# Kernel tuning notes

Hardware: AMD Instinct MI355X
Metric: run time of the kernel (lower is better)

The kernel has to match this reference:

```python
import jax, jax.numpy as jnp
import numpy as np

N_HEADS = 16
ROPE_BASE = 10000.0

def rotate_half(x):
    x1, x2 = jnp.split(x, 2, axis=-1)
    return jnp.concatenate([-x2, x1], axis=-1)

def rope_cos_sin(seq_len, head_dim, dtype):
    inv_freq = 1.0 / (ROPE_BASE ** (jnp.arange(0, head_dim, 2, dtype=jnp.float32) / head_dim))
    t = jnp.arange(seq_len, dtype=jnp.float32)
    freqs = jnp.einsum('i,j->ij', t, inv_freq)           # [S, hd/2]
    emb = jnp.concatenate([freqs, freqs], axis=-1)        # [S, hd]
    return jnp.cos(emb).astype(dtype), jnp.sin(emb).astype(dtype)

def setup_inputs() -> dict:
    key = jax.random.key(0)
    ks = jax.random.split(key, 5)
    B, S, D = 2, 2048, 2048
    x = jax.random.normal(ks[0], (B, S, D), dtype=jnp.float32)
    Wq = jax.random.normal(ks[1], (D, D), dtype=jnp.float32) * (D ** -0.5)
    Wk = jax.random.normal(ks[2], (D, D), dtype=jnp.float32) * (D ** -0.5)
    Wv = jax.random.normal(ks[3], (D, D), dtype=jnp.float32) * (D ** -0.5)
    Wo = jax.random.normal(ks[4], (D, D), dtype=jnp.float32) * (D ** -0.5)
    return {'x': x, 'Wq': Wq, 'Wk': Wk, 'Wv': Wv, 'Wo': Wo}

def reference(x, Wq, Wk, Wv, Wo):
    B, S, D = x.shape
    H = N_HEADS
    hd = D // H
    scale = hd ** -0.5
    # projections (torch Linear: x @ W.T), split heads -> [B, H, S, hd]
    def proj(W):
        return (x @ W.T).reshape(B, S, H, hd).transpose(0, 2, 1, 3)
    q, k, v = proj(Wq), proj(Wk), proj(Wv)
    # RoPE
    cos, sin = rope_cos_sin(S, hd, x.dtype)               # [S, hd]
    cos = cos[None, None, :, :]
    sin = sin[None, None, :, :]
    q = q * cos + rotate_half(q) * sin
    k = k * cos + rotate_half(k) * sin
    # scores + causal mask + fp32 softmax
    scores = jnp.einsum('bhqd,bhkd->bhqk', q, k) * scale
    causal = jnp.triu(jnp.ones((S, S), dtype=bool), k=1)  # True above diag
    scores = jnp.where(causal[None, None, :, :], -jnp.inf, scores)
    attn = jax.nn.softmax(scores.astype(jnp.float32), axis=-1).astype(q.dtype)
    out = jnp.einsum('bhqk,bhkd->bhqd', attn, v)
    out = out.transpose(0, 2, 1, 3).reshape(B, S, D)
    return out @ Wo.T
```

## Files before the change

### kernel.cpp

```cpp
#include <hip/hip_runtime.h>
#include <hip/hip_bf16.h>
#include <math.h>

#define BB 2
#define SS 2048
#define DD 2048
#define HH 16
#define HD 128
#define MM (BB * SS)
#define SCALE 0.08838834764831845f

typedef __attribute__((ext_vector_type(8))) __bf16 bf16x8;
typedef __attribute__((ext_vector_type(4))) float f32x4;
typedef __attribute__((ext_vector_type(8))) unsigned short ushort8v;

__device__ __forceinline__ float bf2f(unsigned short u) {
    union { unsigned int u; float f; } x;
    x.u = ((unsigned int)u) << 16;
    return x.f;
}
__device__ __forceinline__ unsigned short f2bf(float f) {
    union { float f; unsigned int u; } x;
    x.f = f;
    unsigned int r = x.u + 0x7FFFu + ((x.u >> 16) & 1u);
    return (unsigned short)(r >> 16);
}

__global__ __launch_bounds__(256) void cast_f32_bf16(const float* __restrict__ src,
                                                     unsigned short* __restrict__ dst,
                                                     int n4) {
    int i = blockIdx.x * 256 + threadIdx.x;
    if (i >= n4) return;
    float4 v = ((const float4*)src)[i];
    ushort4 o;
    o.x = f2bf(v.x); o.y = f2bf(v.y); o.z = f2bf(v.z); o.w = f2bf(v.w);
    ((ushort4*)dst)[i] = o;
}

__global__ __launch_bounds__(64) void rope_table_kernel(float* __restrict__ cost,
                                                        float* __restrict__ sint) {
    int s = blockIdx.x;
    int i = threadIdx.x;
    float inv = powf(10000.0f, -((float)(2 * i) / 128.0f));
    float ang = (float)s * inv;
    cost[s * 64 + i] = cosf(ang);
    sint[s * 64 + i] = sinf(ang);
}

#define GEMM_BODY(A_, W_, m0_, n0_, K_, ACC_)                                      \
    for (int k0 = 0; k0 < (K_); k0 += 32) {                                        \
        __syncthreads();                                                           \
        _Pragma("unroll")                                                          \
        for (int i = 0; i < 2; ++i) {                                              \
            int c = 2 * w + i;                                                     \
            int row = c * 16 + (l >> 2);                                           \
            const unsigned short* ga = (A_) + (size_t)((m0_) + row) * (K_) + k0 + (l & 3) * 8; \
            __builtin_amdgcn_global_load_lds(                                      \
                (const __attribute__((address_space(1))) unsigned int*)ga,         \
                (__attribute__((address_space(3))) unsigned int*)(As + c * 512),   \
                16, 0, 0);                                                         \
            const unsigned short* gb = (W_) + (size_t)((n0_) + row) * (K_) + k0 + (l & 3) * 8; \
            __builtin_amdgcn_global_load_lds(                                      \
                (const __attribute__((address_space(1))) unsigned int*)gb,         \
                (__attribute__((address_space(3))) unsigned int*)(Bs + c * 512),   \
                16, 0, 0);                                                         \
        }                                                                          \
        __syncthreads();                                                           \
        bf16x8 af[4], bfr[4];                                                      \
        _Pragma("unroll")                                                          \
        for (int i = 0; i < 4; ++i) {                                              \
            af[i]  = *(const bf16x8*)&As[(wr + i * 16 + rlane) * 32 + g * 8];      \
            bfr[i] = *(const bf16x8*)&Bs[(wc + i * 16 + rlane) * 32 + g * 8];      \
        }                                                                          \
        _Pragma("unroll")                                                          \
        for (int i = 0; i < 4; ++i)                                                \
            _Pragma("unroll")                                                      \
            for (int j = 0; j < 4; ++j)                                            \
                ACC_[i][j] = __builtin_amdgcn_mfma_f32_16x16x32_bf16(af[i], bfr[j], ACC_[i][j], 0, 0, 0); \
    }

__global__ __launch_bounds__(256) void gemm_qkv(const unsigned short* __restrict__ A,
                                                const unsigned short* __restrict__ Wc,
                                                unsigned short* __restrict__ qkv) {
    __shared__ unsigned short As[128 * 32];
    __shared__ unsigned short Bs[128 * 32];
    int t = threadIdx.x, w = t >> 6, l = t & 63;
    int rlane = l & 15, g = l >> 4;
    int flat = (int)blockIdx.y * 48 + (int)blockIdx.x;
    int swz = (flat & 7) * 192 + (flat >> 3);
    int n0 = (swz % 48) * 128;
    int m0 = (swz / 48) * 128;
    int wr = (w >> 1) * 64, wc = (w & 1) * 64;
    f32x4 acc[4][4] = {};
    GEMM_BODY(A, Wc, m0, n0, 2048, acc)
    unsigned short* base = qkv + (size_t)(n0 >> 11) * ((size_t)MM * DD);
    int nc0 = n0 & 2047;
#pragma unroll
    for (int i = 0; i < 4; ++i)
#pragma unroll
        for (int r = 0; r < 4; ++r) {
            int row = m0 + wr + i * 16 + g * 4 + r;
#pragma unroll
            for (int j = 0; j < 4; ++j) {
                int col = nc0 + wc + j * 16 + rlane;
                base[(size_t)row * DD + col] = f2bf(acc[i][j][r]);
            }
        }
}

__global__ __launch_bounds__(256) void gemm_out(const unsigned short* __restrict__ A,
                                                const unsigned short* __restrict__ W,
                                                float* __restrict__ C) {
    __shared__ unsigned short As[128 * 32];
    __shared__ unsigned short Bs[128 * 32];
    int t = threadIdx.x, w = t >> 6, l = t & 63;
    int rlane = l & 15, g = l >> 4;
    int flat = (int)blockIdx.y * 16 + (int)blockIdx.x;
    int swz = (flat & 7) * 64 + (flat >> 3);
    int n0 = (swz % 16) * 128;
    int m0 = (swz / 16) * 128;
    int wr = (w >> 1) * 64, wc = (w & 1) * 64;
    f32x4 acc[4][4] = {};
    GEMM_BODY(A, W, m0, n0, 2048, acc)
#pragma unroll
    for (int i = 0; i < 4; ++i)
#pragma unroll
        for (int r = 0; r < 4; ++r) {
            int row = m0 + wr + i * 16 + g * 4 + r;
#pragma unroll
            for (int j = 0; j < 4; ++j) {
                int col = n0 + wc + j * 16 + rlane;
                C[(size_t)row * DD + col] = acc[i][j][r];
            }
        }
}

__global__ __launch_bounds__(256) void rope_apply_kernel(unsigned short* __restrict__ arr,
                                                         const float* __restrict__ cost,
                                                         const float* __restrict__ sint) {
    int idx = blockIdx.x * 256 + threadIdx.x;
    int i4 = (idx & 15) * 4;
    int h = (idx >> 4) & 15;
    int row = idx >> 8;
    int s = row & (SS - 1);
    float4 c  = *(const float4*)&cost[s * 64 + i4];
    float4 sn = *(const float4*)&sint[s * 64 + i4];
    size_t p0 = (size_t)row * DD + h * HD + i4;
    ushort4 lo = *(ushort4*)&arr[p0];
    ushort4 hi = *(ushort4*)&arr[p0 + 64];
    ushort4 olo, ohi;
    olo.x = f2bf(bf2f(lo.x) * c.x - bf2f(hi.x) * sn.x);
    olo.y = f2bf(bf2f(lo.y) * c.y - bf2f(hi.y) * sn.y);
    olo.z = f2bf(bf2f(lo.z) * c.z - bf2f(hi.z) * sn.z);
    olo.w = f2bf(bf2f(lo.w) * c.w - bf2f(hi.w) * sn.w);
    ohi.x = f2bf(bf2f(hi.x) * c.x + bf2f(lo.x) * sn.x);
    ohi.y = f2bf(bf2f(hi.y) * c.y + bf2f(lo.y) * sn.y);
    ohi.z = f2bf(bf2f(hi.z) * c.z + bf2f(lo.z) * sn.z);
    ohi.w = f2bf(bf2f(hi.w) * c.w + bf2f(lo.w) * sn.w);
    *(ushort4*)&arr[p0] = olo;
    *(ushort4*)&arr[p0 + 64] = ohi;
}

__global__ __launch_bounds__(256, 2) void mfma_attn(const unsigned short* __restrict__ qm,
                                                    const unsigned short* __restrict__ km,
                                                    const unsigned short* __restrict__ vm,
                                                    unsigned short* __restrict__ om) {
    __shared__ unsigned short Ks[2][64 * 128];
    __shared__ unsigned short Vt[2][128 * 64];
    __shared__ unsigned short Ps[4][16 * 40];

    int t = threadIdx.x;
    int w = t >> 6;
    int l = t & 63;
    int l15 = l & 15;
    int g = l >> 4;

    int pj = blockIdx.x;
    int h = blockIdx.y;
    int b = blockIdx.z;
    size_t bbase = (size_t)b * SS * DD + (size_t)h * HD;

    int vk0 = 2 * (t >> 3);
    int vd8 = t & 7;
    int cbase = (l15 >> 2) & 3;
    int gsw = (g ^ (l15 & 3)) * 8;

    auto stage_k = [&](int kt2, int buf) {
#pragma unroll
        for (int s = 0; s < 4; ++s) {
            int row = w * 16 + s * 4 + (l >> 4);
            int c = ((l >> 2) & 3) ^ s;
            int gg = (l & 3) ^ (l >> 4);
            const unsigned short* ga = km + bbase +
                (size_t)(kt2 * 64 + row) * DD + c * 32 + gg * 8;
            __builtin_amdgcn_global_load_lds(
                (const __attribute__((address_space(1))) unsigned int*)ga,
                (__attribute__((address_space(3))) unsigned int*)(&Ks[buf][(w * 16 + s * 4) * 128]),
                16, 0, 0);
        }
    };

    ushort8v va[2], vb[2];
    auto load_v = [&](int kt2) {
        const unsigned short* vsrc = vm + bbase + (size_t)(kt2 * 64 + vk0) * DD + vd8 * 8;
        va[0] = *(const ushort8v*)(vsrc);
        vb[0] = *(const ushort8v*)(vsrc + DD);
        va[1] = *(const ushort8v*)(vsrc + 64);
        vb[1] = *(const ushort8v*)(vsrc + DD + 64);
    };
    auto write_v = [&](int buf) {
#pragma unroll
        for (int i = 0; i < 2; ++i)
#pragma unroll
            for (int j = 0; j < 8; ++j) {
                int d = (vd8 + 8 * i) * 8 + j;
                int swz = (vk0 >> 3) ^ ((d >> 3) & 7);
                unsigned int pack = (unsigned int)va[i][j] | ((unsigned int)vb[i][j] << 16);
                *(unsigned int*)&Vt[buf][d * 64 + swz * 8 + (vk0 & 7)] = pack;
            }
    };

#pragma unroll 1
    for (int half = 0; half < 2; ++half) {
        int qt = half ? pj : (31 - pj);
        int q0 = qt * 64;

        bf16x8 qf[4];
        {
            int qrow = q0 + w * 16 + l15;
#pragma unroll
            for (int c = 0; c < 4; ++c)
                qf[c] = *(const bf16x8*)(qm + bbase + (size_t)qrow * DD + c * 32 + g * 8);
        }

        f32x4 acc_o[8] = {};
        float m_ = -INFINITY;
        float l_ = 0.0f;
        int nt = qt + 1;

        stage_k(0, 0);
        load_v(0);
        write_v(0);
        __syncthreads();

        for (int kt = 0; kt < nt; ++kt) {
            int cur = kt & 1;
            bool pref = (kt + 1 < nt);
            if (pref) {
                stage_k(kt + 1, cur ^ 1);
                load_v(kt + 1);
            }

            f32x4 s_[4] = {};
#pragma unroll
            for (int c = 0; c < 4; ++c) {
                int coff = ((c ^ cbase) * 32) + gsw;
#pragma unroll
                for (int kg = 0; kg < 4; ++kg) {
                    bf16x8 kf = *(const bf16x8*)&Ks[cur][(kg * 16 + l15) * 128 + coff];
                    s_[kg] = __builtin_amdgcn_mfma_f32_16x16x32_bf16(kf, qf[c], s_[kg], 0, 0, 0);
                }
            }

            float p[16];
            int qrel = w * 16 + l15;
            bool diag = (kt == qt);
#pragma unroll
            for (int kg = 0; kg < 4; ++kg)
#pragma unroll
                for (int r = 0; r < 4; ++r) {
                    float sv = s_[kg][r] * SCALE;
                    if (diag && (kg * 16 + g * 4 + r > qrel)) sv = -INFINITY;
                    p[kg * 4 + r] = sv;
                }
            float mt01 = fmaxf(fmaxf(p[0], p[1]), fmaxf(p[2], p[3]));
            float mt23 = fmaxf(fmaxf(p[4], p[5]), fmaxf(p[6], p[7]));
            float mt45 = fmaxf(fmaxf(p[8], p[9]), fmaxf(p[10], p[11]));
            float mt67 = fmaxf(fmaxf(p[12], p[13]), fmaxf(p[14], p[15]));
            float mt = fmaxf(fmaxf(mt01, mt23), fmaxf(mt45, mt67));
            mt = fmaxf(mt, __shfl_xor(mt, 16));
            mt = fmaxf(mt, __shfl_xor(mt, 32));
            if (!__all(mt - m_ <= 8.0f)) {
                float mnew = fmaxf(m_, mt);
                float alpha = __expf(m_ - mnew);
                float ar[4];
#pragma unroll
                for (int r = 0; r < 4; ++r) ar[r] = __shfl(alpha, 4 * g + r);
#pragma unroll
                for (int dg = 0; dg < 8; ++dg)
#pragma unroll
                    for (int r = 0; r < 4; ++r) acc_o[dg][r] *= ar[r];
                l_ *= alpha;
                m_ = mnew;
            }
            float ps = 0.0f;
#pragma unroll
            for (int n = 0; n < 16; ++n) {
                p[n] = __expf(p[n] - m_);
                ps += p[n];
            }
            ps += __shfl_xor(ps, 16);
            ps += __shfl_xor(ps, 32);
            l_ += ps;

#pragma unroll
            for (int ks = 0; ks < 2; ++ks) {
#pragma unroll
                for (int kh = 0; kh < 2; ++kh) {
                    int kg = 2 * ks + kh;
                    union { __bf16 hv[4]; uint2 u2; } pk;
#pragma unroll
                    for (int r = 0; r < 4; ++r) pk.hv[r] = (__bf16)p[kg * 4 + r];
                    *(uint2*)&Ps[w][l15 * 40 + kh * 16 + g * 4] = pk.u2;
                }
                bf16x8 pf = *(const bf16x8*)&Ps[w][l15 * 40 + g * 8];
#pragma unroll
                for (int dg = 0; dg < 8; ++dg) {
                    int d = dg * 16 + l15;
                    int swz = (ks * 4 + g) ^ ((d >> 3) & 7);
                    bf16x8 vf = *(const bf16x8*)&Vt[cur][d * 64 + swz * 8];
                    acc_o[dg] = __builtin_amdgcn_mfma_f32_16x16x32_bf16(pf, vf, acc_o[dg], 0, 0, 0);
                }
            }

            if (pref) write_v(cur ^ 1);
            __syncthreads();
        }

        float lr[4];
#pragma unroll
        for (int r = 0; r < 4; ++r) lr[r] = 1.0f / __shfl(l_, 4 * g + r);
#pragma unroll
        for (int dg = 0; dg < 8; ++dg)
#pragma unroll
            for (int r = 0; r < 4; ++r) {
                int qrow2 = q0 + w * 16 + g * 4 + r;
                om[bbase + (size_t)qrow2 * DD + dg * 16 + l15] =
                    f2bf(acc_o[dg][r] * lr[r]);
            }
    }
}

extern "C" void kernel_launch(void* const* d_in, const int* in_sizes, int n_in,
                              void* d_out, int out_size, void* d_ws, size_t ws_size,
                              hipStream_t stream) {
    const float* x  = (const float*)d_in[0];
    const float* Wq = (const float*)d_in[1];
    const float* Wk = (const float*)d_in[2];
    const float* Wv = (const float*)d_in[3];
    const float* Wo = (const float*)d_in[4];
    float* out = (float*)d_out;

    char* ws = (char*)d_ws;
    const size_t MD = (size_t)MM * DD;
    const size_t WN = (size_t)DD * DD;
    unsigned short* qb   = (unsigned short*)(ws);
    unsigned short* kb   = (unsigned short*)(ws + 2 * MD);
    unsigned short* vb   = (unsigned short*)(ws + 4 * MD);
    unsigned short* ctxb = (unsigned short*)(ws + 6 * MD);
    unsigned short* xb   = (unsigned short*)(ws + 8 * MD);
    unsigned short* wqb  = (unsigned short*)(ws + 10 * MD);
    unsigned short* wkb  = (unsigned short*)(ws + 10 * MD + 2 * WN);
    unsigned short* wvb  = (unsigned short*)(ws + 10 * MD + 4 * WN);
    unsigned short* wob  = (unsigned short*)(ws + 10 * MD + 6 * WN);
    float* cost = (float*)(ws + 10 * MD + 8 * WN);
    float* sint = cost + SS * 64;

    cast_f32_bf16<<<(int)(MD / 4 / 256), 256, 0, stream>>>(x, xb, (int)(MD / 4));
    cast_f32_bf16<<<(int)(WN / 4 / 256), 256, 0, stream>>>(Wq, wqb, (int)(WN / 4));
    cast_f32_bf16<<<(int)(WN / 4 / 256), 256, 0, stream>>>(Wk, wkb, (int)(WN / 4));
    cast_f32_bf16<<<(int)(WN / 4 / 256), 256, 0, stream>>>(Wv, wvb, (int)(WN / 4));
    cast_f32_bf16<<<(int)(WN / 4 / 256), 256, 0, stream>>>(Wo, wob, (int)(WN / 4));

    rope_table_kernel<<<SS, 64, 0, stream>>>(cost, sint);

    gemm_qkv<<<dim3(48, 32), 256, 0, stream>>>(xb, wqb, qb);

    rope_apply_kernel<<<2 * MM * HH * 16 / 256, 256, 0, stream>>>(qb, cost, sint);

    mfma_attn<<<dim3(16, HH, BB), 256, 0, stream>>>(qb, kb, vb, ctxb);

    gemm_out<<<dim3(16, 32), 256, 0, stream>>>(ctxb, wob, out);
}
```

Measured before the change: 412.9 us.

## Fuse cast kernels, single-buffer V in attention, raise occupancy, add MFMA priority

The five fp32-to-bf16 cast launches become one kernel that picks source and destination by block index, which removes launch overhead. In the attention kernel the V tile becomes single-buffered to cut LDS use, and launch bounds go from 2 to 3 blocks per SM for more occupancy. s_setprio raises wave priority around the MFMA loops. Single-buffering V adds an extra __syncthreads per iteration before the V write, which serialises the V store behind the PV compute.

```diff
diff --git a/kernel.cpp b/kernel.cpp
--- a/kernel.cpp
+++ b/kernel.cpp
@@ -26,15 +26,30 @@
     return (unsigned short)(r >> 16);
 }
 
-__global__ __launch_bounds__(256) void cast_f32_bf16(const float* __restrict__ src,
-                                                     unsigned short* __restrict__ dst,
-                                                     int n4) {
-    int i = blockIdx.x * 256 + threadIdx.x;
-    if (i >= n4) return;
-    float4 v = ((const float4*)src)[i];
+__global__ __launch_bounds__(256) void cast_all(const float* __restrict__ x,
+                                                const float* __restrict__ Wq,
+                                                const float* __restrict__ Wk,
+                                                const float* __restrict__ Wv,
+                                                const float* __restrict__ Wo,
+                                                unsigned short* __restrict__ xb,
+                                                unsigned short* __restrict__ wqb) {
+    int bid = blockIdx.x;
+    const float* src;
+    unsigned short* dst;
+    int idx;
+    if (bid < 8192) {
+        src = x; dst = xb;
+        idx = bid * 256 + threadIdx.x;
+    } else {
+        int seg = (bid - 8192) >> 12;
+        idx = ((bid - 8192) & 4095) * 256 + threadIdx.x;
+        src = (seg == 0) ? Wq : (seg == 1) ? Wk : (seg == 2) ? Wv : Wo;
+        dst = wqb + (size_t)seg * ((size_t)DD * DD);
+    }
+    float4 v = ((const float4*)src)[idx];
     ushort4 o;
     o.x = f2bf(v.x); o.y = f2bf(v.y); o.z = f2bf(v.z); o.w = f2bf(v.w);
-    ((ushort4*)dst)[i] = o;
+    ((ushort4*)dst)[idx] = o;
 }
 
 __global__ __launch_bounds__(64) void rope_table_kernel(float* __restrict__ cost,
@@ -161,12 +176,12 @@
     *(ushort4*)&arr[p0 + 64] = ohi;
 }
 
-__global__ __launch_bounds__(256, 2) void mfma_attn(const unsigned short* __restrict__ qm,
+__global__ __launch_bounds__(256, 3) void mfma_attn(const unsigned short* __restrict__ qm,
                                                     const unsigned short* __restrict__ km,
                                                     const unsigned short* __restrict__ vm,
                                                     unsigned short* __restrict__ om) {
     __shared__ unsigned short Ks[2][64 * 128];
-    __shared__ unsigned short Vt[2][128 * 64];
+    __shared__ unsigned short Vt[128 * 64];
     __shared__ unsigned short Ps[4][16 * 40];
 
     int t = threadIdx.x;
@@ -208,7 +223,7 @@
         va[1] = *(const ushort8v*)(vsrc + 64);
         vb[1] = *(const ushort8v*)(vsrc + DD + 64);
     };
-    auto write_v = [&](int buf) {
+    auto write_v = [&]() {
 #pragma unroll
         for (int i = 0; i < 2; ++i)
 #pragma unroll
@@ -216,7 +231,7 @@
                 int d = (vd8 + 8 * i) * 8 + j;
                 int swz = (vk0 >> 3) ^ ((d >> 3) & 7);
                 unsigned int pack = (unsigned int)va[i][j] | ((unsigned int)vb[i][j] << 16);
-                *(unsigned int*)&Vt[buf][d * 64 + swz * 8 + (vk0 & 7)] = pack;
+                *(unsigned int*)&Vt[d * 64 + swz * 8 + (vk0 & 7)] = pack;
             }
     };
 
@@ -240,7 +255,7 @@
 
         stage_k(0, 0);
         load_v(0);
-        write_v(0);
+        write_v();
         __syncthreads();
 
         for (int kt = 0; kt < nt; ++kt) {
@@ -252,6 +267,7 @@
             }
 
             f32x4 s_[4] = {};
+            __builtin_amdgcn_s_setprio(1);
 #pragma unroll
             for (int c = 0; c < 4; ++c) {
                 int coff = ((c ^ cbase) * 32) + gsw;
@@ -261,6 +277,7 @@
                     s_[kg] = __builtin_amdgcn_mfma_f32_16x16x32_bf16(kf, qf[c], s_[kg], 0, 0, 0);
                 }
             }
+            __builtin_amdgcn_s_setprio(0);
 
             float p[16];
             int qrel = w * 16 + l15;
@@ -303,6 +320,7 @@
             ps += __shfl_xor(ps, 32);
             l_ += ps;
 
+            __builtin_amdgcn_s_setprio(1);
 #pragma unroll
             for (int ks = 0; ks < 2; ++ks) {
 #pragma unroll
@@ -318,12 +336,14 @@
                 for (int dg = 0; dg < 8; ++dg) {
                     int d = dg * 16 + l15;
                     int swz = (ks * 4 + g) ^ ((d >> 3) & 7);
-                    bf16x8 vf = *(const bf16x8*)&Vt[cur][d * 64 + swz * 8];
+                    bf16x8 vf = *(const bf16x8*)&Vt[d * 64 + swz * 8];
                     acc_o[dg] = __builtin_amdgcn_mfma_f32_16x16x32_bf16(pf, vf, acc_o[dg], 0, 0, 0);
                 }
             }
-
-            if (pref) write_v(cur ^ 1);
+            __builtin_amdgcn_s_setprio(0);
+
+            __syncthreads();
+            if (pref) write_v();
             __syncthreads();
         }
 
@@ -360,17 +380,11 @@
     unsigned short* ctxb = (unsigned short*)(ws + 6 * MD);
     unsigned short* xb   = (unsigned short*)(ws + 8 * MD);
     unsigned short* wqb  = (unsigned short*)(ws + 10 * MD);
-    unsigned short* wkb  = (unsigned short*)(ws + 10 * MD + 2 * WN);
-    unsigned short* wvb  = (unsigned short*)(ws + 10 * MD + 4 * WN);
     unsigned short* wob  = (unsigned short*)(ws + 10 * MD + 6 * WN);
     float* cost = (float*)(ws + 10 * MD + 8 * WN);
     float* sint = cost + SS * 64;
 
-    cast_f32_bf16<<<(int)(MD / 4 / 256), 256, 0, stream>>>(x, xb, (int)(MD / 4));
-    cast_f32_bf16<<<(int)(WN / 4 / 256), 256, 0, stream>>>(Wq, wqb, (int)(WN / 4));
-    cast_f32_bf16<<<(int)(WN / 4 / 256), 256, 0, stream>>>(Wk, wkb, (int)(WN / 4));
-    cast_f32_bf16<<<(int)(WN / 4 / 256), 256, 0, stream>>>(Wv, wvb, (int)(WN / 4));
-    cast_f32_bf16<<<(int)(WN / 4 / 256), 256, 0, stream>>>(Wo, wob, (int)(WN / 4));
+    cast_all<<<8192 + 4 * 4096, 256, 0, stream>>>(x, Wq, Wk, Wv, Wo, xb, wqb);
 
     rope_table_kernel<<<SS, 64, 0, stream>>>(cost, sint);
 
```

Measured after the change: 402.9 us. 2.4% less time.
